# Optimization experiments

Hardware: AMD Instinct MI355X
Metric: run time of the kernel (lower is better)

The kernel has to match this reference:

```python
import jax, jax.numpy as jnp
import numpy as np

B = 8          # batch size (clouds)
NC = 2048      # coarse points per cloud (pos / x)
NF = 8192      # fine points per cloud (pos_skip / x_skip)
C = 256        # coarse feature dim
CS = 64        # skip feature dim
OUT = 256      # MLP output dim
K = 3          # knn_interpolate k (FPParams default)
EPS = 1e-16    # PyG clamp epsilon on squared distance


def setup_inputs() -> dict:
    key = jax.random.key(0)
    ks = jax.random.split(key, 8)
    x = jax.random.normal(ks[0], (B * NC, C), dtype=jnp.float32)
    pos = jax.random.normal(ks[1], (B * NC, 3), dtype=jnp.float32)
    x_skip = jax.random.normal(ks[2], (B * NF, CS), dtype=jnp.float32)
    pos_skip = jax.random.normal(ks[3], (B * NF, 3), dtype=jnp.float32)
    # contiguous, sorted batch assignments (standard PyG layout)
    batch = jnp.repeat(jnp.arange(B, dtype=jnp.int64), NC)
    batch_skip = jnp.repeat(jnp.arange(B, dtype=jnp.int64), NF)
    W1 = jax.random.normal(ks[4], (C + CS, OUT), dtype=jnp.float32) * (1.0 / np.sqrt(C + CS))
    b1 = jnp.zeros((OUT,), dtype=jnp.float32)
    W2 = jax.random.normal(ks[5], (OUT, OUT), dtype=jnp.float32) * (1.0 / np.sqrt(OUT))
    b2 = jnp.zeros((OUT,), dtype=jnp.float32)
    return {"x": x, "pos": pos, "batch": batch, "x_skip": x_skip,
            "pos_skip": pos_skip, "batch_skip": batch_skip,
            "W1": W1, "b1": b1, "W2": W2, "b2": b2}


def _knn_interpolate(x, pos, pos_skip):
    # x: [B*NC, C], pos: [B*NC, 3], pos_skip: [B*NF, 3]
    posb = pos.reshape(B, NC, 3)
    posf = pos_skip.reshape(B, NF, 3)
    xb = x.reshape(B, NC, -1)
    # squared pairwise distances per cloud: [B, NF, NC]
    d2 = jnp.sum((posf[:, :, None, :] - posb[:, None, :, :]) ** 2, axis=-1)
    neg_d2, idx = jax.lax.top_k(-d2, K)          # k nearest -> [B, NF, K]
    d2k = -neg_d2
    w = 1.0 / jnp.maximum(d2k, EPS)              # inverse squared-distance weights
    w = w / jnp.sum(w, axis=-1, keepdims=True)   # [B, NF, K]
    gathered = jax.vmap(lambda xv, iv: xv[iv])(xb, idx)  # [B, NF, K, C]
    out = jnp.sum(gathered * w[..., None], axis=2)       # [B, NF, C]
    return out.reshape(B * NF, -1)


def reference(x, pos, batch, x_skip, pos_skip, batch_skip, W1, b1, W2, b2):
    # 1) interpolate coarse features onto fine points (pos.shape[0] != pos_skip.shape[0])
    xi = _knn_interpolate(x, pos, pos_skip)        # [B*NF, C]
    # 2) concat skip features
    h = jnp.concatenate([xi, x_skip], axis=1)      # [B*NF, C+CS]
    # 3) MLP: Linear -> ReLU -> Linear -> ReLU
    h = jax.nn.relu(h @ W1 + b1)
    h = jax.nn.relu(h @ W2 + b2)
    return (h, pos_skip, batch_skip)
```

## Files before the change

### kernel.cpp

```cpp
#include <hip/hip_runtime.h>
#include <hip/hip_bf16.h>

#define BATCH 8
#define NC 2048
#define NF 8192
#define CDIM 256
#define CSKIP 64
#define OUTD 256
#define MTOT (BATCH*NF)
#define NCTOT (BATCH*NC)
#define NCHUNK 8
#define CHSZ (NC/NCHUNK)

typedef __attribute__((ext_vector_type(8))) short short8;
typedef __attribute__((ext_vector_type(4))) float floatx4;

static __device__ __forceinline__ ushort f2bf(float f) {
    union { float f; unsigned u; } v; v.f = f;
    unsigned r = v.u + 0x7fffu + ((v.u >> 16) & 1u);
    return (ushort)(r >> 16);
}
static __device__ __forceinline__ float bf2f(ushort u) {
    union { unsigned u; float f; } v; v.u = ((unsigned)u) << 16;
    return v.f;
}

#if defined(__has_builtin) && __has_builtin(__builtin_amdgcn_fmed3f)
#define MED3F(a, b, c) __builtin_amdgcn_fmed3f((a), (b), (c))
#else
static __device__ __forceinline__ float MED3F(float a, float b, float c) {
    return fmaxf(fminf(a, b), fminf(fmaxf(a, b), c));
}
#endif

#define TOP3_INSERT(d, jj)                          \
    {                                               \
        bool c2 = (d) < d2, c1 = (d) < d1, c0 = (d) < d0; \
        i2 = c1 ? i1 : (c2 ? (jj) : i2);            \
        i1 = c0 ? i0 : (c1 ? (jj) : i1);            \
        i0 = c0 ? (jj) : i0;                        \
        d2 = MED3F(d1, d2, (d));                    \
        d1 = MED3F(d0, d1, (d));                    \
        d0 = fminf(d0, (d));                        \
    }

#define SEG0 1048576
#define SEG1 1048576
#define SEG2 65536
#define SEG3 16384
#define SEG4 65536
#define SEG5 16384
#define SEG6 (MTOT*3)
#define SEG7 MTOT
#define PREP_THREADS (SEG0+SEG1+SEG2+SEG3+SEG4+SEG5+SEG6+SEG7)

__global__ __launch_bounds__(256) void prep_kernel(const float* __restrict__ x,
                                                   const float* __restrict__ x_skip,
                                                   const float* __restrict__ W1,
                                                   const float* __restrict__ W2,
                                                   const float* __restrict__ pos,
                                                   const float* __restrict__ pos_skip,
                                                   ushort* __restrict__ xb,
                                                   ushort* __restrict__ xsb,
                                                   ushort* __restrict__ Bt1a,
                                                   ushort* __restrict__ Bt1b,
                                                   ushort* __restrict__ Bt2,
                                                   float4* __restrict__ pos4,
                                                   float* __restrict__ out) {
    int t = blockIdx.x * 256 + threadIdx.x;
    if (t < SEG0) {
        float4 v = ((const float4*)x)[t];
        ushort4 p; p.x = f2bf(v.x); p.y = f2bf(v.y); p.z = f2bf(v.z); p.w = f2bf(v.w);
        ((ushort4*)xb)[t] = p;
        return;
    }
    t -= SEG0;
    if (t < SEG1) {
        float4 v = ((const float4*)x_skip)[t];
        ushort4 p; p.x = f2bf(v.x); p.y = f2bf(v.y); p.z = f2bf(v.z); p.w = f2bf(v.w);
        ((ushort4*)xsb)[t] = p;
        return;
    }
    t -= SEG1;
    if (t < SEG2) {
        int k = t & 255, n = t >> 8;
        Bt1a[n * 256 + k] = f2bf(W1[k * 256 + n]);
        return;
    }
    t -= SEG2;
    if (t < SEG3) {
        int k2 = t & 63, n = t >> 6;
        Bt1b[n * 64 + k2] = f2bf(W1[(256 + k2) * 256 + n]);
        return;
    }
    t -= SEG3;
    if (t < SEG4) {
        int k = t & 255, n = t >> 8;
        Bt2[n * 256 + k] = f2bf(W2[k * 256 + n]);
        return;
    }
    t -= SEG4;
    if (t < SEG5) {
        float4 q;
        q.x = pos[t * 3 + 0]; q.y = pos[t * 3 + 1]; q.z = pos[t * 3 + 2]; q.w = 0.f;
        pos4[t] = q;
        return;
    }
    t -= SEG5;
    if (t < SEG6) {
        out[(size_t)MTOT * OUTD + t] = pos_skip[t];
        return;
    }
    t -= SEG6;
    if (t < SEG7) {
        out[(size_t)MTOT * OUTD + (size_t)MTOT * 3 + t] = (float)(t >> 13);
    }
}

__global__ __launch_bounds__(256) void knn_part(const float4* __restrict__ pos4,
                                                const float* __restrict__ pos_skip,
                                                int* __restrict__ pidx,
                                                float* __restrict__ pdst) {
    __shared__ float sx[CHSZ], sy[CHSZ], sz[CHSZ];
    int c = blockIdx.x & (NCHUNK - 1);
    int m = (blockIdx.x >> 3) * 256 + threadIdx.x;
    int b = m >> 13;
    int jbase = b * NC + c * CHSZ;

    float4 q0 = pos4[jbase + threadIdx.x];
    sx[threadIdx.x] = q0.x; sy[threadIdx.x] = q0.y; sz[threadIdx.x] = q0.z;
    float px = pos_skip[m * 3 + 0];
    float py = pos_skip[m * 3 + 1];
    float pz = pos_skip[m * 3 + 2];
    __syncthreads();

    float d0 = 1e30f, d1 = 1e30f, d2 = 1e30f;
    int i0 = jbase, i1 = jbase, i2 = jbase;
#pragma unroll 2
    for (int j4 = 0; j4 < CHSZ; j4 += 4) {
        float4 qx = *(const float4*)&sx[j4];
        float4 qy = *(const float4*)&sy[j4];
        float4 qz = *(const float4*)&sz[j4];
#pragma unroll
        for (int u = 0; u < 4; ++u) {
            float dx = px - qx[u], dy = py - qy[u], dz = pz - qz[u];
            float d = dx * dx + dy * dy + dz * dz;
            int jj = jbase + j4 + u;
            TOP3_INSERT(d, jj);
        }
    }
    size_t base = ((size_t)c * MTOT + m) * 3;
    pdst[base + 0] = d0; pdst[base + 1] = d1; pdst[base + 2] = d2;
    pidx[base + 0] = i0; pidx[base + 1] = i1; pidx[base + 2] = i2;
}

__global__ __launch_bounds__(64) void knn_merge(const int* __restrict__ pidx,
                                                const float* __restrict__ pdst,
                                                int* __restrict__ idxw,
                                                float* __restrict__ wgt) {
    int m = blockIdx.x * 64 + threadIdx.x;
    float d0 = 1e30f, d1 = 1e30f, d2 = 1e30f;
    int i0 = 0, i1 = 0, i2 = 0;
#pragma unroll
    for (int c = 0; c < NCHUNK; ++c) {
        size_t base = ((size_t)c * MTOT + m) * 3;
#pragma unroll
        for (int s = 0; s < 3; ++s) {
            float d = pdst[base + s];
            int jj = pidx[base + s];
            TOP3_INSERT(d, jj);
        }
    }
    float w0 = 1.0f / fmaxf(d0, 1e-16f);
    float w1 = 1.0f / fmaxf(d1, 1e-16f);
    float w2 = 1.0f / fmaxf(d2, 1e-16f);
    float inv = 1.0f / (w0 + w1 + w2);
    idxw[m * 3 + 0] = i0;  wgt[m * 3 + 0] = w0 * inv;
    idxw[m * 3 + 1] = i1;  wgt[m * 3 + 1] = w1 * inv;
    idxw[m * 3 + 2] = i2;  wgt[m * 3 + 2] = w2 * inv;
}

__global__ __launch_bounds__(256) void gemm_G(const ushort* __restrict__ A,
                                              const ushort* __restrict__ Bt,
                                              ushort* __restrict__ Gb) {
    int wave = threadIdx.x >> 6, lane = threadIdx.x & 63;
    int m0 = blockIdx.x * 16;
    int lrow = lane & 15;
    int ko = (lane >> 4) * 8;
    const ushort* arow = A + (size_t)(m0 + lrow) * 256 + ko;
    const ushort* bbase = Bt + (size_t)(wave * 64 + lrow) * 256 + ko;

    floatx4 acc[4];
#pragma unroll
    for (int i = 0; i < 4; ++i) acc[i] = (floatx4){0.f, 0.f, 0.f, 0.f};

    for (int k0 = 0; k0 < 256; k0 += 32) {
        short8 af = *(const short8*)(arow + k0);
#pragma unroll
        for (int nt = 0; nt < 4; ++nt) {
            short8 bf = *(const short8*)(bbase + (size_t)nt * 16 * 256 + k0);
            acc[nt] = __builtin_amdgcn_mfma_f32_16x16x32_bf16(af, bf, acc[nt], 0, 0, 0);
        }
    }
    int rbase = (lane >> 4) * 4;
#pragma unroll
    for (int nt = 0; nt < 4; ++nt) {
        int n = wave * 64 + nt * 16 + lrow;
#pragma unroll
        for (int r = 0; r < 4; ++r)
            Gb[(size_t)(m0 + rbase + r) * 256 + n] = f2bf(acc[nt][r]);
    }
}

#define LDS_STRIDE 264
#define WB_STRIDE 72
__global__ __launch_bounds__(256) void fused_kernel(const ushort* __restrict__ xsb,
                                                    const ushort* __restrict__ Bt1b,
                                                    const ushort* __restrict__ Gb,
                                                    const int* __restrict__ idxw,
                                                    const float* __restrict__ wgt,
                                                    const float* __restrict__ b1,
                                                    const ushort* __restrict__ Bt2,
                                                    const float* __restrict__ b2,
                                                    float* __restrict__ out) {
    __shared__ ushort h1t[4][16 * LDS_STRIDE];
    __shared__ ushort wB[256 * WB_STRIDE];
    __shared__ int   sIdx[4][48];
    __shared__ float sWgt[4][48];
    int tid = threadIdx.x;
    int wave = tid >> 6, lane = tid & 63;
    int m0 = blockIdx.x * 64 + wave * 16;
    int lrow = lane & 15;
    int ko = (lane >> 4) * 8;
    int rbase = (lane >> 4) * 4;

    if (lane < 48) {
        sIdx[wave][lane] = idxw[m0 * 3 + lane];
        sWgt[wave][lane] = wgt[m0 * 3 + lane];
    }

    const ushort4* Gv = (const ushort4*)Gb;
    const int*   si = sIdx[wave];
    const float* sw = sWgt[wave];
    ushort4 g[4][3];
#define GATHER(slot, i) {                                         \
        int a0 = si[(i) * 3 + 0];                                 \
        int a1 = si[(i) * 3 + 1];                                 \
        int a2 = si[(i) * 3 + 2];                                 \
        g[slot][0] = Gv[(size_t)a0 * 64 + lane];                  \
        g[slot][1] = Gv[(size_t)a1 * 64 + lane];                  \
        g[slot][2] = Gv[(size_t)a2 * 64 + lane]; }

    GATHER(0, 0) GATHER(1, 1) GATHER(2, 2) GATHER(3, 3)

    for (int cch = tid; cch < 2048; cch += 256) {
        int n = cch >> 3, koff = (cch & 7) * 8;
        *(short8*)&wB[n * WB_STRIDE + koff] = *(const short8*)(Bt1b + n * 64 + koff);
    }
    __syncthreads();

    floatx4 acc[16];
#pragma unroll
    for (int i = 0; i < 16; ++i) acc[i] = (floatx4){0.f, 0.f, 0.f, 0.f};
    {
        const ushort* arow = xsb + (size_t)(m0 + lrow) * 64 + ko;
#pragma unroll
        for (int k0 = 0; k0 < 64; k0 += 32) {
            short8 af = *(const short8*)(arow + k0);
#pragma unroll
            for (int nt = 0; nt < 16; ++nt) {
                short8 bf = *(const short8*)&wB[(nt * 16 + lrow) * WB_STRIDE + k0 + ko];
                acc[nt] = __builtin_amdgcn_mfma_f32_16x16x32_bf16(af, bf, acc[nt], 0, 0, 0);
            }
        }
    }

    ushort* ht = h1t[wave];
#pragma unroll
    for (int nt = 0; nt < 16; ++nt) {
        int n = nt * 16 + lrow;
#pragma unroll
        for (int r = 0; r < 4; ++r)
            ht[(rbase + r) * LDS_STRIDE + n] = f2bf(acc[nt][r]);
    }

    {
        float4 bv = ((const float4*)b1)[lane];
#define COMBINE(i) {                                              \
        int s = (i) & 3;                                          \
        float w0 = sw[(i) * 3 + 0], w1 = sw[(i) * 3 + 1], w2 = sw[(i) * 3 + 2]; \
        ushort4 sv = *(const ushort4*)(ht + (i) * LDS_STRIDE + 4 * lane); \
        float4 h;                                                 \
        h.x = fmaxf(bf2f(sv.x) + w0 * bf2f(g[s][0].x) + w1 * bf2f(g[s][1].x) + w2 * bf2f(g[s][2].x) + bv.x, 0.f); \
        h.y = fmaxf(bf2f(sv.y) + w0 * bf2f(g[s][0].y) + w1 * bf2f(g[s][1].y) + w2 * bf2f(g[s][2].y) + bv.y, 0.f); \
        h.z = fmaxf(bf2f(sv.z) + w0 * bf2f(g[s][0].z) + w1 * bf2f(g[s][1].z) + w2 * bf2f(g[s][2].z) + bv.z, 0.f); \
        h.w = fmaxf(bf2f(sv.w) + w0 * bf2f(g[s][0].w) + w1 * bf2f(g[s][1].w) + w2 * bf2f(g[s][2].w) + bv.w, 0.f); \
        ushort4 hp;                                               \
        hp.x = f2bf(h.x); hp.y = f2bf(h.y); hp.z = f2bf(h.z); hp.w = f2bf(h.w); \
        *(ushort4*)(ht + (i) * LDS_STRIDE + 4 * lane) = hp; }

#pragma unroll
        for (int i = 0; i < 12; ++i) { COMBINE(i); GATHER(i & 3, i + 4); }
#pragma unroll
        for (int i = 12; i < 16; ++i) { COMBINE(i); }
#undef GATHER
#undef COMBINE
    }

#pragma unroll
    for (int i = 0; i < 16; ++i) acc[i] = (floatx4){0.f, 0.f, 0.f, 0.f};
    for (int s = 0; s < 4; ++s) {
        __syncthreads();
        for (int cch = tid; cch < 2048; cch += 256) {
            int n = cch >> 3, koff = (cch & 7) * 8;
            *(short8*)&wB[n * WB_STRIDE + koff] = *(const short8*)(Bt2 + n * 256 + s * 64 + koff);
        }
        __syncthreads();
        const ushort* ar = ht + lrow * LDS_STRIDE + s * 64 + ko;
#pragma unroll
        for (int k0 = 0; k0 < 64; k0 += 32) {
            short8 af = *(const short8*)(ar + k0);
#pragma unroll
            for (int nt = 0; nt < 16; ++nt) {
                short8 bf = *(const short8*)&wB[(nt * 16 + lrow) * WB_STRIDE + k0 + ko];
                acc[nt] = __builtin_amdgcn_mfma_f32_16x16x32_bf16(af, bf, acc[nt], 0, 0, 0);
            }
        }
    }
#pragma unroll
    for (int nt = 0; nt < 16; ++nt) {
        int n = nt * 16 + lrow;
        float bv2 = b2[n];
#pragma unroll
        for (int r = 0; r < 4; ++r) {
            float v = fmaxf(acc[nt][r] + bv2, 0.f);
            out[(size_t)(m0 + rbase + r) * OUTD + n] = v;
        }
    }
}

extern "C" void kernel_launch(void* const* d_in, const int* in_sizes, int n_in,
                              void* d_out, int out_size, void* d_ws, size_t ws_size,
                              hipStream_t stream) {
    const float* x        = (const float*)d_in[0];
    const float* pos      = (const float*)d_in[1];
    const float* x_skip   = (const float*)d_in[3];
    const float* pos_skip = (const float*)d_in[4];
    const float* W1       = (const float*)d_in[6];
    const float* b1       = (const float*)d_in[7];
    const float* W2       = (const float*)d_in[8];
    const float* b2       = (const float*)d_in[9];

    char* ws = (char*)d_ws;
    size_t off = 0;
    int*    idxw = (int*)(ws + off);    off += (size_t)MTOT * 3 * 4;
    float*  wgt  = (float*)(ws + off);  off += (size_t)MTOT * 3 * 4;
    ushort* xb   = (ushort*)(ws + off); off += (size_t)NCTOT * 256 * 2;
    ushort* xsb  = (ushort*)(ws + off); off += (size_t)MTOT * 64 * 2;
    ushort* Gb   = (ushort*)(ws + off); off += (size_t)NCTOT * 256 * 2;
    ushort* Bt1a = (ushort*)(ws + off); off += (size_t)256 * 256 * 2;
    ushort* Bt1b = (ushort*)(ws + off); off += (size_t)256 * 64 * 2;
    ushort* Bt2  = (ushort*)(ws + off); off += (size_t)256 * 256 * 2;
    float4* pos4 = (float4*)(ws + off); off += (size_t)(NCTOT + 4) * 16;
    float* out = (float*)d_out;
    int*   pidx = (int*)d_out;
    float* pdst = (float*)((char*)d_out + (size_t)NCHUNK * MTOT * 3 * 4);

    prep_kernel<<<(PREP_THREADS + 255) / 256, 256, 0, stream>>>(
        x, x_skip, W1, W2, pos, pos_skip, xb, xsb, Bt1a, Bt1b, Bt2, pos4, out);
    knn_part<<<(MTOT / 256) * NCHUNK, 256, 0, stream>>>(pos4, pos_skip, pidx, pdst);
    knn_merge<<<MTOT / 64, 64, 0, stream>>>(pidx, pdst, idxw, wgt);
    gemm_G<<<NCTOT / 16, 256, 0, stream>>>(xb, Bt1a, Gb);
    fused_kernel<<<MTOT / 64, 256, 0, stream>>>(xsb, Bt1b, Gb, idxw, wgt, b1, Bt2, b2, out);
}
```

Before: 229.3 us.

## Tile weight transpose, process two queries per kNN thread, stage GEMM weights in LDS

```diff
diff --git a/kernel.cpp b/kernel.cpp
--- a/kernel.cpp
+++ b/kernel.cpp
@@ -33,38 +33,30 @@
 }
 #endif
 
-#define TOP3_INSERT(d, jj)                          \
+#define TOP3_INS(d, jj, D0, D1, D2, I0, I1, I2)     \
     {                                               \
-        bool c2 = (d) < d2, c1 = (d) < d1, c0 = (d) < d0; \
-        i2 = c1 ? i1 : (c2 ? (jj) : i2);            \
-        i1 = c0 ? i0 : (c1 ? (jj) : i1);            \
-        i0 = c0 ? (jj) : i0;                        \
-        d2 = MED3F(d1, d2, (d));                    \
-        d1 = MED3F(d0, d1, (d));                    \
-        d0 = fminf(d0, (d));                        \
+        bool c2 = (d) < D2, c1 = (d) < D1, c0 = (d) < D0; \
+        I2 = c1 ? I1 : (c2 ? (jj) : I2);            \
+        I1 = c0 ? I0 : (c1 ? (jj) : I1);            \
+        I0 = c0 ? (jj) : I0;                        \
+        D2 = MED3F(D1, D2, (d));                    \
+        D1 = MED3F(D0, D1, (d));                    \
+        D0 = fminf(D0, (d));                        \
     }
 
 #define SEG0 1048576
 #define SEG1 1048576
-#define SEG2 65536
-#define SEG3 16384
-#define SEG4 65536
 #define SEG5 16384
 #define SEG6 (MTOT*3)
 #define SEG7 MTOT
-#define PREP_THREADS (SEG0+SEG1+SEG2+SEG3+SEG4+SEG5+SEG6+SEG7)
+#define PREP_THREADS (SEG0+SEG1+SEG5+SEG6+SEG7)
 
 __global__ __launch_bounds__(256) void prep_kernel(const float* __restrict__ x,
                                                    const float* __restrict__ x_skip,
-                                                   const float* __restrict__ W1,
-                                                   const float* __restrict__ W2,
                                                    const float* __restrict__ pos,
                                                    const float* __restrict__ pos_skip,
                                                    ushort* __restrict__ xb,
                                                    ushort* __restrict__ xsb,
-                                                   ushort* __restrict__ Bt1a,
-                                                   ushort* __restrict__ Bt1b,
-                                                   ushort* __restrict__ Bt2,
                                                    float4* __restrict__ pos4,
                                                    float* __restrict__ out) {
     int t = blockIdx.x * 256 + threadIdx.x;
@@ -82,24 +74,6 @@
         return;
     }
     t -= SEG1;
-    if (t < SEG2) {
-        int k = t & 255, n = t >> 8;
-        Bt1a[n * 256 + k] = f2bf(W1[k * 256 + n]);
-        return;
-    }
-    t -= SEG2;
-    if (t < SEG3) {
-        int k2 = t & 63, n = t >> 6;
-        Bt1b[n * 64 + k2] = f2bf(W1[(256 + k2) * 256 + n]);
-        return;
-    }
-    t -= SEG3;
-    if (t < SEG4) {
-        int k = t & 255, n = t >> 8;
-        Bt2[n * 256 + k] = f2bf(W2[k * 256 + n]);
-        return;
-    }
-    t -= SEG4;
     if (t < SEG5) {
         float4 q;
         q.x = pos[t * 3 + 0]; q.y = pos[t * 3 + 1]; q.z = pos[t * 3 + 2]; q.w = 0.f;
@@ -114,6 +88,31 @@
     t -= SEG6;
     if (t < SEG7) {
         out[(size_t)MTOT * OUTD + (size_t)MTOT * 3 + t] = (float)(t >> 13);
+    }
+}
+
+__global__ __launch_bounds__(256) void prep_w(const float* __restrict__ W1,
+                                              const float* __restrict__ W2,
+                                              ushort* __restrict__ Bt1a,
+                                              ushort* __restrict__ Bt1b,
+                                              ushort* __restrict__ Bt2) {
+    __shared__ ushort tile[64 * 65];
+    int bid = blockIdx.x;
+    const float* src; ushort* dst; int k0, n0, KD;
+    if (bid < 16)      { src = W1;             dst = Bt1a; k0 = (bid >> 2) * 64; n0 = (bid & 3) * 64; KD = 256; }
+    else if (bid < 20) { src = W1 + 256 * 256; dst = Bt1b; k0 = 0;               n0 = (bid - 16) * 64; KD = 64; }
+    else               { int b2 = bid - 20; src = W2; dst = Bt2; k0 = (b2 >> 2) * 64; n0 = (b2 & 3) * 64; KD = 256; }
+    int tx = threadIdx.x & 63, ty = threadIdx.x >> 6;
+#pragma unroll
+    for (int r = 0; r < 64; r += 4) {
+        int k = r + ty;
+        tile[k * 65 + tx] = f2bf(src[(size_t)(k0 + k) * 256 + n0 + tx]);
+    }
+    __syncthreads();
+#pragma unroll
+    for (int r = 0; r < 64; r += 4) {
+        int n = r + ty;
+        dst[(size_t)(n0 + n) * KD + k0 + tx] = tile[tx * 65 + n];
     }
 }
 
@@ -123,19 +122,25 @@
                                                 float* __restrict__ pdst) {
     __shared__ float sx[CHSZ], sy[CHSZ], sz[CHSZ];
     int c = blockIdx.x & (NCHUNK - 1);
-    int m = (blockIdx.x >> 3) * 256 + threadIdx.x;
-    int b = m >> 13;
+    int mA = (blockIdx.x >> 3) * 512 + threadIdx.x;
+    int mB = mA + 256;
+    int b = mA >> 13;
     int jbase = b * NC + c * CHSZ;
 
     float4 q0 = pos4[jbase + threadIdx.x];
     sx[threadIdx.x] = q0.x; sy[threadIdx.x] = q0.y; sz[threadIdx.x] = q0.z;
-    float px = pos_skip[m * 3 + 0];
-    float py = pos_skip[m * 3 + 1];
-    float pz = pos_skip[m * 3 + 2];
+    float pxA = pos_skip[mA * 3 + 0];
+    float pyA = pos_skip[mA * 3 + 1];
+    float pzA = pos_skip[mA * 3 + 2];
+    float pxB = pos_skip[mB * 3 + 0];
+    float pyB = pos_skip[mB * 3 + 1];
+    float pzB = pos_skip[mB * 3 + 2];
     __syncthreads();
 
-    float d0 = 1e30f, d1 = 1e30f, d2 = 1e30f;
-    int i0 = jbase, i1 = jbase, i2 = jbase;
+    float dA0 = 1e30f, dA1 = 1e30f, dA2 = 1e30f;
+    float dB0 = 1e30f, dB1 = 1e30f, dB2 = 1e30f;
+    int iA0 = jbase, iA1 = jbase, iA2 = jbase;
+    int iB0 = jbase, iB1 = jbase, iB2 = jbase;
 #pragma unroll 2
     for (int j4 = 0; j4 < CHSZ; j4 += 4) {
         float4 qx = *(const float4*)&sx[j4];
@@ -143,15 +148,21 @@
         float4 qz = *(const float4*)&sz[j4];
 #pragma unroll
         for (int u = 0; u < 4; ++u) {
-            float dx = px - qx[u], dy = py - qy[u], dz = pz - qz[u];
-            float d = dx * dx + dy * dy + dz * dz;
             int jj = jbase + j4 + u;
-            TOP3_INSERT(d, jj);
-        }
-    }
-    size_t base = ((size_t)c * MTOT + m) * 3;
-    pdst[base + 0] = d0; pdst[base + 1] = d1; pdst[base + 2] = d2;
-    pidx[base + 0] = i0; pidx[base + 1] = i1; pidx[base + 2] = i2;
+            float ax = pxA - qx[u], ay = pyA - qy[u], az = pzA - qz[u];
+            float dA = ax * ax + ay * ay + az * az;
+            TOP3_INS(dA, jj, dA0, dA1, dA2, iA0, iA1, iA2);
+            float bx = pxB - qx[u], by = pyB - qy[u], bz = pzB - qz[u];
+            float dB = bx * bx + by * by + bz * bz;
+            TOP3_INS(dB, jj, dB0, dB1, dB2, iB0, iB1, iB2);
+        }
+    }
+    size_t baseA = ((size_t)c * MTOT + mA) * 3;
+    pdst[baseA + 0] = dA0; pdst[baseA + 1] = dA1; pdst[baseA + 2] = dA2;
+    pidx[baseA + 0] = iA0; pidx[baseA + 1] = iA1; pidx[baseA + 2] = iA2;
+    size_t baseB = ((size_t)c * MTOT + mB) * 3;
+    pdst[baseB + 0] = dB0; pdst[baseB + 1] = dB1; pdst[baseB + 2] = dB2;
+    pidx[baseB + 0] = iB0; pidx[baseB + 1] = iB1; pidx[baseB + 2] = iB2;
 }
 
 __global__ __launch_bounds__(64) void knn_merge(const int* __restrict__ pidx,
@@ -168,7 +179,7 @@
         for (int s = 0; s < 3; ++s) {
             float d = pdst[base + s];
             int jj = pidx[base + s];
-            TOP3_INSERT(d, jj);
+            TOP3_INS(d, jj, d0, d1, d2, i0, i1, i2);
         }
     }
     float w0 = 1.0f / fmaxf(d0, 1e-16f);
@@ -180,32 +191,43 @@
     idxw[m * 3 + 2] = i2;  wgt[m * 3 + 2] = w2 * inv;
 }
 
+#define GW_STRIDE 72
 __global__ __launch_bounds__(256) void gemm_G(const ushort* __restrict__ A,
                                               const ushort* __restrict__ Bt,
                                               ushort* __restrict__ Gb) {
-    int wave = threadIdx.x >> 6, lane = threadIdx.x & 63;
-    int m0 = blockIdx.x * 16;
+    __shared__ ushort wB[256 * GW_STRIDE];
+    int tid = threadIdx.x;
+    int wave = tid >> 6, lane = tid & 63;
+    int m0 = blockIdx.x * 64 + wave * 16;
     int lrow = lane & 15;
     int ko = (lane >> 4) * 8;
-    const ushort* arow = A + (size_t)(m0 + lrow) * 256 + ko;
-    const ushort* bbase = Bt + (size_t)(wave * 64 + lrow) * 256 + ko;
-
-    floatx4 acc[4];
-#pragma unroll
-    for (int i = 0; i < 4; ++i) acc[i] = (floatx4){0.f, 0.f, 0.f, 0.f};
-
-    for (int k0 = 0; k0 < 256; k0 += 32) {
-        short8 af = *(const short8*)(arow + k0);
-#pragma unroll
-        for (int nt = 0; nt < 4; ++nt) {
-            short8 bf = *(const short8*)(bbase + (size_t)nt * 16 * 256 + k0);
-            acc[nt] = __builtin_amdgcn_mfma_f32_16x16x32_bf16(af, bf, acc[nt], 0, 0, 0);
+
+    floatx4 acc[16];
+#pragma unroll
+    for (int i = 0; i < 16; ++i) acc[i] = (floatx4){0.f, 0.f, 0.f, 0.f};
+
+    for (int s = 0; s < 4; ++s) {
+        if (s) __syncthreads();
+        for (int cch = tid; cch < 2048; cch += 256) {
+            int n = cch >> 3, koff = (cch & 7) * 8;
+            *(short8*)&wB[n * GW_STRIDE + koff] = *(const short8*)(Bt + n * 256 + s * 64 + koff);
+        }
+        __syncthreads();
+        const ushort* ar = A + (size_t)(m0 + lrow) * 256 + s * 64 + ko;
+#pragma unroll
+        for (int k0 = 0; k0 < 64; k0 += 32) {
+            short8 af = *(const short8*)(ar + k0);
+#pragma unroll
+            for (int nt = 0; nt < 16; ++nt) {
+                short8 bf = *(const short8*)&wB[(nt * 16 + lrow) * GW_STRIDE + k0 + ko];
+                acc[nt] = __builtin_amdgcn_mfma_f32_16x16x32_bf16(af, bf, acc[nt], 0, 0, 0);
+            }
         }
     }
     int rbase = (lane >> 4) * 4;
 #pragma unroll
-    for (int nt = 0; nt < 4; ++nt) {
-        int n = wave * 64 + nt * 16 + lrow;
+    for (int nt = 0; nt < 16; ++nt) {
+        int n = nt * 16 + lrow;
 #pragma unroll
         for (int r = 0; r < 4; ++r)
             Gb[(size_t)(m0 + rbase + r) * 256 + n] = f2bf(acc[nt][r]);
@@ -367,9 +389,10 @@
     float* pdst = (float*)((char*)d_out + (size_t)NCHUNK * MTOT * 3 * 4);
 
     prep_kernel<<<(PREP_THREADS + 255) / 256, 256, 0, stream>>>(
-        x, x_skip, W1, W2, pos, pos_skip, xb, xsb, Bt1a, Bt1b, Bt2, pos4, out);
-    knn_part<<<(MTOT / 256) * NCHUNK, 256, 0, stream>>>(pos4, pos_skip, pidx, pdst);
+        x, x_skip, pos, pos_skip, xb, xsb, pos4, out);
+    prep_w<<<36, 256, 0, stream>>>(W1, W2, Bt1a, Bt1b, Bt2);
+    knn_part<<<(MTOT / 512) * NCHUNK, 256, 0, stream>>>(pos4, pos_skip, pidx, pdst);
     knn_merge<<<MTOT / 64, 64, 0, stream>>>(pidx, pdst, idxw, wgt);
-    gemm_G<<<NCTOT / 16, 256, 0, stream>>>(xb, Bt1a, Gb);
+    gemm_G<<<NCTOT / 64, 256, 0, stream>>>(xb, Bt1a, Gb);
     fused_kernel<<<MTOT / 64, 256, 0, stream>>>(xsb, Bt1b, Gb, idxw, wgt, b1, Bt2, b2, out);
 }
```

Result: no change. 226.2 us (-1.3%).
